# Kernel tuning notes

Measured on AMD Instinct MI355X. Metric: run time of the kernel, lower is better.

The kernel has to match this reference:

```python
import jax, jax.numpy as jnp
import numpy as np

KH = KW = 3
SH = SW = 1
PH = PW = 1
EPS = 1e-6


def _unfold(x, kh, kw, sh, sw, ph, pw):
    """Replicates torch.nn.functional.unfold: returns [B, C*kh*kw, L]."""
    x = jnp.pad(x, ((0, 0), (0, 0), (ph, ph), (pw, pw)))
    B, C, H, W = x.shape
    Ho = (H - kh) // sh + 1
    Wo = (W - kw) // sw + 1
    # channel-major, then (kh, kw) ordering, matching F.unfold
    cols = jnp.stack(
        [x[:, :, i:i + (Ho - 1) * sh + 1:sh, j:j + (Wo - 1) * sw + 1:sw]
         for i in range(kh) for j in range(kw)],
        axis=2,
    )  # [B, C, kh*kw, Ho, Wo]
    return cols.reshape(B, C * kh * kw, Ho * Wo), Ho, Wo


def setup_inputs() -> dict:
    key = jax.random.key(0)
    k1, k2, k3 = jax.random.split(key, 3)
    x = jax.random.normal(k1, (4, 32, 32, 32), dtype=jnp.float32)
    positions = jax.random.uniform(k2, (32, 32, 3, 3, 5), dtype=jnp.float32,
                                   minval=-1.0, maxval=1.0)
    values = jax.random.normal(k3, (32, 32, 3, 3, 5), dtype=jnp.float32) * 0.01
    return {"x": x, "positions": positions, "values": values}


def _piecewise_conv(x, positions, values):
    O, C, kh, kw, P = positions.shape
    patches, Ho, Wo = _unfold(x, KH, KW, SH, SW, PH, PW)  # [B, T, L]
    T = C * kh * kw
    B = x.shape[0]
    L = Ho * Wo

    pos = positions.reshape(O, T, P)
    val = values.reshape(O, T, P)
    # forward sorts each (out_ch, input) table by position
    order = jnp.argsort(pos, axis=-1)
    pos = jnp.take_along_axis(pos, order, axis=-1)
    val = jnp.take_along_axis(val, order, axis=-1)

    xv = patches.transpose(0, 2, 1)          # [B, L, T]
    xb = xv[:, None, :, :]                   # [B, 1, L, T]

    # interval index: last j with pos[j] <= x (== count(pos <= x) - 1)
    cnt = jnp.sum(pos[None, :, None, :, :] <= xb[..., None], axis=-1)  # [B,O,L,T]
    idx = jnp.clip(cnt - 1, 0, P - 2)

    def gather(tab, ind):
        # tab: [O, T, P], ind: [B, O, L, T] -> [B, O, L, T]
        ind2 = ind.transpose(1, 3, 0, 2).reshape(O, T, B * L)
        out = jnp.take_along_axis(tab, ind2, axis=-1)
        return out.reshape(O, T, B, L).transpose(2, 0, 3, 1)

    pos_j = gather(pos, idx)
    pos_j1 = gather(pos, idx + 1)
    val_j = gather(val, idx)
    val_j1 = gather(val, idx + 1)

    t = jnp.clip((xb - pos_j) / (pos_j1 - pos_j + EPS), 0.0, 1.0)
    interp = val_j + t * (val_j1 - val_j)
    res = jnp.where(pos_j == pos_j1, val_j, interp)

    first = pos[None, :, None, :, 0]
    last = pos[None, :, None, :, P - 1]
    v0 = val[None, :, None, :, 0]
    vl = val[None, :, None, :, P - 1]
    res = jnp.where(xb <= first, v0, jnp.where(xb >= last, vl, res))

    out = res.sum(axis=-1)                   # [B, O, L]
    return out.reshape(B, O, Ho, Wo)


def reference(x, positions, values):
    return _piecewise_conv(x, positions, values)
```

## Files before the change

### kernel.cpp

```cpp
#include <hip/hip_runtime.h>

#define B_  4
#define O_  32
#define C_  32
#define H_  32
#define W_  32
#define P_  5
#define T_  288
#define PIX (H_ * W_)
#define EPSF 1e-6f

#define NCH 2
#define CG  (C_ / NCH)


__global__ __launch_bounds__(256) void prep_tables(
    const float* __restrict__ pos, const float* __restrict__ val,
    float* __restrict__ tab)
{
    int id = blockIdx.x * 256 + threadIdx.x;
    if (id >= O_ * T_) return;

    const float* pp = pos + id * P_;
    const float* vv = val + id * P_;
    float p0 = pp[0], p1 = pp[1], p2 = pp[2], p3 = pp[3], p4 = pp[4];
    float v0 = vv[0], v1 = vv[1], v2 = vv[2], v3 = vv[3], v4 = vv[4];

#define CSWAP(a, b, va, vb)                         \
    {                                               \
        float _pa = fminf(a, b), _pb = fmaxf(a, b); \
        bool _sw = (a > b);                         \
        float _va = _sw ? vb : va;                  \
        float _vb = _sw ? va : vb;                  \
        a = _pa; b = _pb; va = _va; vb = _vb;       \
    }
    CSWAP(p0, p1, v0, v1);
    CSWAP(p3, p4, v3, v4);
    CSWAP(p2, p4, v2, v4);
    CSWAP(p2, p3, v2, v3);
    CSWAP(p1, p4, v1, v4);
    CSWAP(p0, p3, v0, v3);
    CSWAP(p0, p2, v0, v2);
    CSWAP(p1, p3, v1, v3);
    CSWAP(p1, p2, v1, v2);
#undef CSWAP

    float inv0 = 1.0f / (p1 - p0 + EPSF);
    float inv1 = 1.0f / (p2 - p1 + EPSF);
    float inv2 = 1.0f / (p3 - p2 + EPSF);
    float inv3 = 1.0f / (p4 - p3 + EPSF);

    float* e = tab + id * 16;
    e[0]  = inv0;        e[1]  = inv1;        e[2]  = inv2;        e[3]  = inv3;
    e[4]  = -p0 * inv0;  e[5]  = -p1 * inv1;  e[6]  = -p2 * inv2;  e[7]  = -p3 * inv3;
    e[8]  = v1 - v0;     e[9]  = v2 - v1;     e[10] = v3 - v2;     e[11] = v4 - v3;
    e[12] = v0;          e[13] = 0.f;         e[14] = 0.f;         e[15] = 0.f;
}

#define XROW 34
#define XSTR 35
#define XS_PER_CH (XROW * XSTR)
#define TABF (NCH * 9 * 16)

__global__ __launch_bounds__(256, 4) void pw_conv(
    const float* __restrict__ x, const float* __restrict__ tab,
    float* __restrict__ part)
{
    __shared__ float xs[NCH * XS_PER_CH];
    __shared__ float ts[TABF];

    const int cg = blockIdx.x;
    const int o  = blockIdx.y;
    const int b  = blockIdx.z;
    const int tid = threadIdx.x;
    const int c0 = cg * NCH;

    const float* tg = tab + (o * T_ + c0 * 9) * 16;
    for (int i = tid; i < TABF; i += 256) ts[i] = tg[i];

    const float* xb = x + (b * C_ + c0) * PIX;
    for (int idx = tid; idx < NCH * XROW * XROW; idx += 256) {
        int ch  = idx / (XROW * XROW);
        int rem = idx - ch * (XROW * XROW);
        int r   = rem / XROW;
        int col = rem - r * XROW;
        int gr = r - 1, gc = col - 1;
        float v = 0.f;
        if ((unsigned)gr < (unsigned)H_ && (unsigned)gc < (unsigned)W_)
            v = xb[ch * PIX + gr * W_ + gc];
        xs[ch * XS_PER_CH + r * XSTR + col] = v;
    }
    __syncthreads();

    const int r  = tid >> 3;
    const int c4 = (tid & 7) * 4;

    float acc0 = 0.f, acc1 = 0.f, acc2 = 0.f, acc3 = 0.f;

#pragma unroll
    for (int ch = 0; ch < NCH; ++ch) {
        float xr[3][6];
#pragma unroll
        for (int i = 0; i < 3; ++i)
#pragma unroll
            for (int j = 0; j < 6; ++j)
                xr[i][j] = xs[ch * XS_PER_CH + (r + i) * XSTR + c4 + j];

        const float4* e4 = (const float4*)(ts + ch * 9 * 16);
#pragma unroll
        for (int ij = 0; ij < 9; ++ij) {
            const int i = ij / 3, j = ij % 3;
            const float4 qi = e4[ij * 4 + 0];
            const float4 qf = e4[ij * 4 + 1];
            const float4 qd = e4[ij * 4 + 2];
            const float  v0 = e4[ij * 4 + 3].x;

#define EVAL(ACC, XV)                                                        \
            {                                                                \
                float _xv = (XV);                                            \
                ACC += v0;                                                   \
                float _t;                                                    \
                _t = fmaf(_xv, qi.x, qf.x);                                  \
                _t = fminf(fmaxf(_t, 0.f), 1.f); ACC = fmaf(_t, qd.x, ACC);  \
                _t = fmaf(_xv, qi.y, qf.y);                                  \
                _t = fminf(fmaxf(_t, 0.f), 1.f); ACC = fmaf(_t, qd.y, ACC);  \
                _t = fmaf(_xv, qi.z, qf.z);                                  \
                _t = fminf(fmaxf(_t, 0.f), 1.f); ACC = fmaf(_t, qd.z, ACC);  \
                _t = fmaf(_xv, qi.w, qf.w);                                  \
                _t = fminf(fmaxf(_t, 0.f), 1.f); ACC = fmaf(_t, qd.w, ACC);  \
            }
            EVAL(acc0, xr[i][j + 0]);
            EVAL(acc1, xr[i][j + 1]);
            EVAL(acc2, xr[i][j + 2]);
            EVAL(acc3, xr[i][j + 3]);
#undef EVAL
        }
    }

    float4 res; res.x = acc0; res.y = acc1; res.z = acc2; res.w = acc3;
    float4* pp = (float4*)(part + ((size_t)(cg * B_ + b) * O_ + o) * PIX);
    pp[tid] = res;
}

__global__ __launch_bounds__(256) void reduce16(
    const float* __restrict__ part, float* __restrict__ out)
{
    int j = blockIdx.x * 256 + threadIdx.x;
    const float4* p4 = (const float4*)part;
    float4 s; s.x = 0.f; s.y = 0.f; s.z = 0.f; s.w = 0.f;
#pragma unroll
    for (int cg = 0; cg < CG; ++cg) {
        float4 p = p4[cg * (B_ * O_ * PIX / 4) + j];
        s.x += p.x; s.y += p.y; s.z += p.z; s.w += p.w;
    }
    ((float4*)out)[j] = s;
}

extern "C" void kernel_launch(void* const* d_in, const int* in_sizes, int n_in,
                              void* d_out, int out_size, void* d_ws, size_t ws_size,
                              hipStream_t stream)
{
    const float* x   = (const float*)d_in[0];
    const float* pos = (const float*)d_in[1];
    const float* val = (const float*)d_in[2];

    float* tab  = (float*)d_ws;
    float* part = (float*)((char*)d_ws + (1 << 20));

    prep_tables<<<(O_ * T_ + 255) / 256, 256, 0, stream>>>(pos, val, tab);

    dim3 grid(CG, O_, B_);
    pw_conv<<<grid, 256, 0, stream>>>(x, tab, part);

    int n4 = B_ * O_ * PIX / 4;
    reduce16<<<n4 / 256, 256, 0, stream>>>(part, (float*)d_out);
}
```

Before: 77.02 us.

## Fuse table prep into conv kernel and process two output channels per block

```diff
diff --git a/kernel.cpp b/kernel.cpp
--- a/kernel.cpp
+++ b/kernel.cpp
@@ -12,71 +12,70 @@
 
 #define NCH 2
 #define CG  (C_ / NCH)
+#define NO  2
+#define OG  (O_ / NO)
 
-
-__global__ __launch_bounds__(256) void prep_tables(
-    const float* __restrict__ pos, const float* __restrict__ val,
-    float* __restrict__ tab)
-{
-    int id = blockIdx.x * 256 + threadIdx.x;
-    if (id >= O_ * T_) return;
-
-    const float* pp = pos + id * P_;
-    const float* vv = val + id * P_;
-    float p0 = pp[0], p1 = pp[1], p2 = pp[2], p3 = pp[3], p4 = pp[4];
-    float v0 = vv[0], v1 = vv[1], v2 = vv[2], v3 = vv[3], v4 = vv[4];
-
-#define CSWAP(a, b, va, vb)                         \
-    {                                               \
-        float _pa = fminf(a, b), _pb = fmaxf(a, b); \
-        bool _sw = (a > b);                         \
-        float _va = _sw ? vb : va;                  \
-        float _vb = _sw ? va : vb;                  \
-        a = _pa; b = _pb; va = _va; vb = _vb;       \
-    }
-    CSWAP(p0, p1, v0, v1);
-    CSWAP(p3, p4, v3, v4);
-    CSWAP(p2, p4, v2, v4);
-    CSWAP(p2, p3, v2, v3);
-    CSWAP(p1, p4, v1, v4);
-    CSWAP(p0, p3, v0, v3);
-    CSWAP(p0, p2, v0, v2);
-    CSWAP(p1, p3, v1, v3);
-    CSWAP(p1, p2, v1, v2);
-#undef CSWAP
-
-    float inv0 = 1.0f / (p1 - p0 + EPSF);
-    float inv1 = 1.0f / (p2 - p1 + EPSF);
-    float inv2 = 1.0f / (p3 - p2 + EPSF);
-    float inv3 = 1.0f / (p4 - p3 + EPSF);
-
-    float* e = tab + id * 16;
-    e[0]  = inv0;        e[1]  = inv1;        e[2]  = inv2;        e[3]  = inv3;
-    e[4]  = -p0 * inv0;  e[5]  = -p1 * inv1;  e[6]  = -p2 * inv2;  e[7]  = -p3 * inv3;
-    e[8]  = v1 - v0;     e[9]  = v2 - v1;     e[10] = v3 - v2;     e[11] = v4 - v3;
-    e[12] = v0;          e[13] = 0.f;         e[14] = 0.f;         e[15] = 0.f;
-}
+#define ENT (NO * NCH * 9)
+#define TABF (ENT * 16)
 
 #define XROW 34
 #define XSTR 35
 #define XS_PER_CH (XROW * XSTR)
-#define TABF (NCH * 9 * 16)
 
 __global__ __launch_bounds__(256, 4) void pw_conv(
-    const float* __restrict__ x, const float* __restrict__ tab,
-    float* __restrict__ part)
+    const float* __restrict__ x, const float* __restrict__ pos,
+    const float* __restrict__ val, float* __restrict__ part)
 {
     __shared__ float xs[NCH * XS_PER_CH];
     __shared__ float ts[TABF];
 
     const int cg = blockIdx.x;
-    const int o  = blockIdx.y;
+    const int og = blockIdx.y;
     const int b  = blockIdx.z;
     const int tid = threadIdx.x;
     const int c0 = cg * NCH;
+    const int o0 = og * NO;
 
-    const float* tg = tab + (o * T_ + c0 * 9) * 16;
-    for (int i = tid; i < TABF; i += 256) ts[i] = tg[i];
+    if (tid < ENT) {
+        const int oo = tid / (NCH * 9);
+        const int rem = tid - oo * (NCH * 9);
+        const int id = (o0 + oo) * T_ + c0 * 9 + rem;
+
+        const float* pp = pos + id * P_;
+        const float* vv = val + id * P_;
+        float p0 = pp[0], p1 = pp[1], p2 = pp[2], p3 = pp[3], p4 = pp[4];
+        float v0 = vv[0], v1 = vv[1], v2 = vv[2], v3 = vv[3], v4 = vv[4];
+
+#define CSWAP(a, bb, va, vb)                        \
+        {                                           \
+            float _pa = fminf(a, bb), _pb = fmaxf(a, bb); \
+            bool _sw = (a > bb);                    \
+            float _va = _sw ? vb : va;              \
+            float _vb = _sw ? va : vb;              \
+            a = _pa; bb = _pb; va = _va; vb = _vb;  \
+        }
+        CSWAP(p0, p1, v0, v1);
+        CSWAP(p3, p4, v3, v4);
+        CSWAP(p2, p4, v2, v4);
+        CSWAP(p2, p3, v2, v3);
+        CSWAP(p1, p4, v1, v4);
+        CSWAP(p0, p3, v0, v3);
+        CSWAP(p0, p2, v0, v2);
+        CSWAP(p1, p3, v1, v3);
+        CSWAP(p1, p2, v1, v2);
+#undef CSWAP
+
+        float inv0 = 1.0f / (p1 - p0 + EPSF);
+        float inv1 = 1.0f / (p2 - p1 + EPSF);
+        float inv2 = 1.0f / (p3 - p2 + EPSF);
+        float inv3 = 1.0f / (p4 - p3 + EPSF);
+
+        float* e = ts + tid * 16;
+        e[0]  = inv0;        e[1]  = inv1;        e[2]  = inv2;        e[3]  = inv3;
+        e[4]  = -p0 * inv0;  e[5]  = -p1 * inv1;  e[6]  = -p2 * inv2;  e[7]  = -p3 * inv3;
+        e[8]  = v1 - v0;     e[9]  = v2 - v1;     e[10] = v3 - v2;     e[11] = v4 - v3;
+        e[12] = v0;          e[13] = 0.f;         e[14] = 0.f;         e[15] = 0.f;
+    }
 
     const float* xb = x + (b * C_ + c0) * PIX;
     for (int idx = tid; idx < NCH * XROW * XROW; idx += 256) {
@@ -95,7 +94,7 @@
     const int r  = tid >> 3;
     const int c4 = (tid & 7) * 4;
 
-    float acc0 = 0.f, acc1 = 0.f, acc2 = 0.f, acc3 = 0.f;
+    float acc[NO][4] = {{0.f, 0.f, 0.f, 0.f}, {0.f, 0.f, 0.f, 0.f}};
 
 #pragma unroll
     for (int ch = 0; ch < NCH; ++ch) {
@@ -106,40 +105,48 @@
             for (int j = 0; j < 6; ++j)
                 xr[i][j] = xs[ch * XS_PER_CH + (r + i) * XSTR + c4 + j];
 
-        const float4* e4 = (const float4*)(ts + ch * 9 * 16);
 #pragma unroll
-        for (int ij = 0; ij < 9; ++ij) {
-            const int i = ij / 3, j = ij % 3;
-            const float4 qi = e4[ij * 4 + 0];
-            const float4 qf = e4[ij * 4 + 1];
-            const float4 qd = e4[ij * 4 + 2];
-            const float  v0 = e4[ij * 4 + 3].x;
+        for (int oo = 0; oo < NO; ++oo) {
+            const float4* e4 = (const float4*)(ts + (oo * NCH + ch) * 9 * 16);
+#pragma unroll
+            for (int ij = 0; ij < 9; ++ij) {
+                const int i = ij / 3, j = ij % 3;
+                const float4 qi = e4[ij * 4 + 0];
+                const float4 qf = e4[ij * 4 + 1];
+                const float4 qd = e4[ij * 4 + 2];
+                const float  v0 = e4[ij * 4 + 3].x;
 
 #define EVAL(ACC, XV)                                                        \
-            {                                                                \
-                float _xv = (XV);                                            \
-                ACC += v0;                                                   \
-                float _t;                                                    \
-                _t = fmaf(_xv, qi.x, qf.x);                                  \
-                _t = fminf(fmaxf(_t, 0.f), 1.f); ACC = fmaf(_t, qd.x, ACC);  \
-                _t = fmaf(_xv, qi.y, qf.y);                                  \
-                _t = fminf(fmaxf(_t, 0.f), 1.f); ACC = fmaf(_t, qd.y, ACC);  \
-                _t = fmaf(_xv, qi.z, qf.z);                                  \
-                _t = fminf(fmaxf(_t, 0.f), 1.f); ACC = fmaf(_t, qd.z, ACC);  \
-                _t = fmaf(_xv, qi.w, qf.w);                                  \
-                _t = fminf(fmaxf(_t, 0.f), 1.f); ACC = fmaf(_t, qd.w, ACC);  \
+                {                                                            \
+                    float _xv = (XV);                                        \
+                    ACC += v0;                                               \
+                    float _t;                                                \
+                    _t = fmaf(_xv, qi.x, qf.x);                              \
+                    _t = fminf(fmaxf(_t, 0.f), 1.f); ACC = fmaf(_t, qd.x, ACC); \
+                    _t = fmaf(_xv, qi.y, qf.y);                              \
+                    _t = fminf(fmaxf(_t, 0.f), 1.f); ACC = fmaf(_t, qd.y, ACC); \
+                    _t = fmaf(_xv, qi.z, qf.z);                              \
+                    _t = fminf(fmaxf(_t, 0.f), 1.f); ACC = fmaf(_t, qd.z, ACC); \
+                    _t = fmaf(_xv, qi.w, qf.w);                              \
+                    _t = fminf(fmaxf(_t, 0.f), 1.f); ACC = fmaf(_t, qd.w, ACC); \
+                }
+                EVAL(acc[oo][0], xr[i][j + 0]);
+                EVAL(acc[oo][1], xr[i][j + 1]);
+                EVAL(acc[oo][2], xr[i][j + 2]);
+                EVAL(acc[oo][3], xr[i][j + 3]);
+#undef EVAL
             }
-            EVAL(acc0, xr[i][j + 0]);
-            EVAL(acc1, xr[i][j + 1]);
-            EVAL(acc2, xr[i][j + 2]);
-            EVAL(acc3, xr[i][j + 3]);
-#undef EVAL
         }
     }
 
-    float4 res; res.x = acc0; res.y = acc1; res.z = acc2; res.w = acc3;
-    float4* pp = (float4*)(part + ((size_t)(cg * B_ + b) * O_ + o) * PIX);
-    pp[tid] = res;
+#pragma unroll
+    for (int oo = 0; oo < NO; ++oo) {
+        float4 res;
+        res.x = acc[oo][0]; res.y = acc[oo][1];
+        res.z = acc[oo][2]; res.w = acc[oo][3];
+        float4* pp = (float4*)(part + ((size_t)(cg * B_ + b) * O_ + o0 + oo) * PIX);
+        pp[tid] = res;
+    }
 }
 
 __global__ __launch_bounds__(256) void reduce16(
@@ -164,13 +171,10 @@
     const float* pos = (const float*)d_in[1];
     const float* val = (const float*)d_in[2];
 
-    float* tab  = (float*)d_ws;
-    float* part = (float*)((char*)d_ws + (1 << 20));
+    float* part = (float*)d_ws;
 
-    prep_tables<<<(O_ * T_ + 255) / 256, 256, 0, stream>>>(pos, val, tab);
-
-    dim3 grid(CG, O_, B_);
-    pw_conv<<<grid, 256, 0, stream>>>(x, tab, part);
+    dim3 grid(CG, OG, B_);
+    pw_conv<<<grid, 256, 0, stream>>>(x, pos, val, part);
 
     int n4 = B_ * O_ * PIX / 4;
     reduce16<<<n4 / 256, 256, 0, stream>>>(part, (float*)d_out);
```

After: 75.02 us. 2.6% less time.
